# Optimization experiments

Hardware: AMD Instinct MI355X
Metric: run time of the kernel (lower is better)

Reference implementation:

```python
import jax, jax.numpy as jnp
from jax import lax
import numpy as np

B, C, H, W = 32, 1, 224, 224
F, KS = 64, 7

def setup_inputs() -> dict:
    key = jax.random.key(0)
    k1, k2 = jax.random.split(key)
    x = jax.random.normal(k1, (B, C, H, W), dtype=jnp.float32)
    # torch.rand -> uniform [0,1)
    kernel = jax.random.uniform(k2, (F, KS, KS), dtype=jnp.float32)
    return {"input": x, "kernel": kernel}

def reference(input, kernel):
    # Original: zero-pad by k//2 on all sides, then for each output pixel
    # out[b, f, i, j] = sum(patch[b, 0] * kernel[f]) -> single-input-channel conv.
    ks = kernel.shape[-1]
    pad = ks // 2
    w = kernel[:, None, :, :]  # [F, 1, ks, ks] in OIHW
    out = lax.conv_general_dilated(
        input, w,
        window_strides=(1, 1),
        padding=[(pad, pad), (pad, pad)],
        dimension_numbers=("NCHW", "OIHW", "NCHW"),
    )
    return out  # [B, F, H, W]
```

## Files before the change

kernel.cpp:

```cpp
#include <hip/hip_runtime.h>


#define TILE   32
#define HALO   3
#define LTILE  (TILE + 2 * HALO)
#define H_     224
#define W_     224
#define B_     32
#define F_     64
#define KS_    7

__global__ __launch_bounds__(256)
void Conv_58394375356438_kernel(const float* __restrict__ in,
                                const float* __restrict__ wt,
                                float* __restrict__ out)
{
    __shared__ float tile[LTILE * LTILE];

    const int blk = blockIdx.x;
    const int tx  = blk % (W_ / TILE);
    const int ty  = (blk / (W_ / TILE)) % (H_ / TILE);
    const int b   = blk / ((W_ / TILE) * (H_ / TILE));

    const int x0 = tx * TILE;
    const int y0 = ty * TILE;
    const float* __restrict__ inp = in + b * (H_ * W_);

    for (int i = threadIdx.x; i < LTILE * LTILE; i += 256) {
        const int ly = i / LTILE;
        const int lx = i - ly * LTILE;
        const int gy = y0 + ly - HALO;
        const int gx = x0 + lx - HALO;
        float v = 0.0f;
        if (gy >= 0 && gy < H_ && gx >= 0 && gx < W_)
            v = inp[gy * W_ + gx];
        tile[i] = v;
    }
    __syncthreads();

    const int r  = threadIdx.x >> 3;
    const int cx = (threadIdx.x & 7) * 4;

    float patch[KS_][10];
    #pragma unroll
    for (int ky = 0; ky < KS_; ++ky) {
        #pragma unroll
        for (int kx = 0; kx < 10; ++kx) {
            patch[ky][kx] = tile[(r + ky) * LTILE + cx + kx];
        }
    }

    float* __restrict__ outp = out + ((size_t)(b * F_) * H_ + (y0 + r)) * W_ + (x0 + cx);

    #pragma unroll 2
    for (int f = 0; f < F_; ++f) {
        const float* __restrict__ wf = wt + f * (KS_ * KS_);
        float acc0 = 0.0f, acc1 = 0.0f, acc2 = 0.0f, acc3 = 0.0f;
        #pragma unroll
        for (int ky = 0; ky < KS_; ++ky) {
            #pragma unroll
            for (int kx = 0; kx < KS_; ++kx) {
                const float w = wf[ky * KS_ + kx];
                acc0 = fmaf(patch[ky][kx + 0], w, acc0);
                acc1 = fmaf(patch[ky][kx + 1], w, acc1);
                acc2 = fmaf(patch[ky][kx + 2], w, acc2);
                acc3 = fmaf(patch[ky][kx + 3], w, acc3);
            }
        }
        float4 v = make_float4(acc0, acc1, acc2, acc3);
        *reinterpret_cast<float4*>(outp + (size_t)f * (H_ * W_)) = v;
    }
}

extern "C" void kernel_launch(void* const* d_in, const int* in_sizes, int n_in,
                              void* d_out, int out_size, void* d_ws, size_t ws_size,
                              hipStream_t stream)
{
    const float* in = (const float*)d_in[0];
    const float* wt = (const float*)d_in[1];
    float* out      = (float*)d_out;

    const int grid = B_ * (H_ / TILE) * (W_ / TILE);
    Conv_58394375356438_kernel<<<grid, 256, 0, stream>>>(in, wt, out);
}
```

Measured before the change: 527.3 us.

## Use fp16 dot2 packed MACs with LDS weights and split filters across blocks

After: 442.0 us. 16.2% less time.

```diff
diff --git a/kernel.cpp b/kernel.cpp
--- a/kernel.cpp
+++ b/kernel.cpp
@@ -1,34 +1,50 @@
 #include <hip/hip_runtime.h>
 
 
-#define TILE   32
-#define HALO   3
-#define LTILE  (TILE + 2 * HALO)
-#define H_     224
-#define W_     224
-#define B_     32
-#define F_     64
-#define KS_    7
+#define TILE    32
+#define HALO    3
+#define LTY     (TILE + 2 * HALO)
+#define LTX     40
+#define H_      224
+#define W_      224
+#define B_      32
+#define F_      64
+#define FB_     32
+#define KS_     7
+
+typedef _Float16 half2_t __attribute__((ext_vector_type(2)));
+
+__device__ __forceinline__ float dot2(half2_t a, half2_t b, float c) {
+#if __has_builtin(__builtin_amdgcn_fdot2)
+    return __builtin_amdgcn_fdot2(a, b, c, false);
+#else
+    return c + (float)a.x * (float)b.x + (float)a.y * (float)b.y;
+#endif
+}
 
 __global__ __launch_bounds__(256)
 void Conv_58394375356438_kernel(const float* __restrict__ in,
                                 const float* __restrict__ wt,
                                 float* __restrict__ out)
 {
-    __shared__ float tile[LTILE * LTILE];
+    __shared__ float   tile[LTY * LTX];
+    __shared__ half2_t w2lds[FB_ * 32];
 
-    const int blk = blockIdx.x;
-    const int tx  = blk % (W_ / TILE);
-    const int ty  = (blk / (W_ / TILE)) % (H_ / TILE);
-    const int b   = blk / ((W_ / TILE) * (H_ / TILE));
+    const int blk   = blockIdx.x;
+    const int fhalf = blk & 1;
+    const int rest  = blk >> 1;
+    const int tx    = rest % (W_ / TILE);
+    const int ty    = (rest / (W_ / TILE)) % (H_ / TILE);
+    const int b     = rest / ((W_ / TILE) * (H_ / TILE));
 
     const int x0 = tx * TILE;
     const int y0 = ty * TILE;
+    const int fb = fhalf * FB_;
     const float* __restrict__ inp = in + b * (H_ * W_);
 
-    for (int i = threadIdx.x; i < LTILE * LTILE; i += 256) {
-        const int ly = i / LTILE;
-        const int lx = i - ly * LTILE;
+    for (int i = threadIdx.x; i < LTY * LTX; i += 256) {
+        const int ly = i / LTX;
+        const int lx = i - ly * LTX;
         const int gy = y0 + ly - HALO;
         const int gx = x0 + lx - HALO;
         float v = 0.0f;
@@ -36,38 +52,60 @@
             v = inp[gy * W_ + gx];
         tile[i] = v;
     }
+
+    for (int idx = threadIdx.x; idx < FB_ * 28; idx += 256) {
+        const int f   = idx / 28;
+        const int t   = idx - f * 28;
+        const int row = t >> 2;
+        const int j   = t & 3;
+        const int kx  = 2 * j;
+        const float* wg = wt + (fb + f) * (KS_ * KS_) + row * KS_ + kx;
+        const float w0 = wg[0];
+        const float w1 = (kx + 1 < KS_) ? wg[1] : 0.0f;
+        half2_t h;
+        h.x = (_Float16)w0;
+        h.y = (_Float16)w1;
+        w2lds[f * 32 + t] = h;
+    }
     __syncthreads();
 
     const int r  = threadIdx.x >> 3;
     const int cx = (threadIdx.x & 7) * 4;
 
-    float patch[KS_][10];
+    half2_t pairs[KS_][10];
     #pragma unroll
     for (int ky = 0; ky < KS_; ++ky) {
+        const int base = (r + ky) * LTX + cx;
+        float c[11];
         #pragma unroll
-        for (int kx = 0; kx < 10; ++kx) {
-            patch[ky][kx] = tile[(r + ky) * LTILE + cx + kx];
+        for (int s = 0; s < 11; ++s) c[s] = tile[base + s];
+        #pragma unroll
+        for (int s = 0; s < 10; ++s) {
+            half2_t h;
+            h.x = (_Float16)c[s];
+            h.y = (_Float16)c[s + 1];
+            pairs[ky][s] = h;
         }
     }
 
-    float* __restrict__ outp = out + ((size_t)(b * F_) * H_ + (y0 + r)) * W_ + (x0 + cx);
+    float* __restrict__ outp =
+        out + ((size_t)(b * F_ + fb) * H_ + (y0 + r)) * W_ + (x0 + cx);
 
-    #pragma unroll 2
-    for (int f = 0; f < F_; ++f) {
-        const float* __restrict__ wf = wt + f * (KS_ * KS_);
-        float acc0 = 0.0f, acc1 = 0.0f, acc2 = 0.0f, acc3 = 0.0f;
+    for (int f = 0; f < FB_; ++f) {
+        const half2_t* __restrict__ wf = &w2lds[f * 32];
+        float a0 = 0.0f, a1 = 0.0f, a2 = 0.0f, a3 = 0.0f;
         #pragma unroll
         for (int ky = 0; ky < KS_; ++ky) {
             #pragma unroll
-            for (int kx = 0; kx < KS_; ++kx) {
-                const float w = wf[ky * KS_ + kx];
-                acc0 = fmaf(patch[ky][kx + 0], w, acc0);
-                acc1 = fmaf(patch[ky][kx + 1], w, acc1);
-                acc2 = fmaf(patch[ky][kx + 2], w, acc2);
-                acc3 = fmaf(patch[ky][kx + 3], w, acc3);
+            for (int j = 0; j < 4; ++j) {
+                const half2_t w = wf[ky * 4 + j];
+                a0 = dot2(pairs[ky][0 + 2 * j], w, a0);
+                a1 = dot2(pairs[ky][1 + 2 * j], w, a1);
+                a2 = dot2(pairs[ky][2 + 2 * j], w, a2);
+                a3 = dot2(pairs[ky][3 + 2 * j], w, a3);
             }
         }
-        float4 v = make_float4(acc0, acc1, acc2, acc3);
+        float4 v = make_float4(a0, a1, a2, a3);
         *reinterpret_cast<float4*>(outp + (size_t)f * (H_ * W_)) = v;
     }
 }
@@ -80,6 +118,6 @@
     const float* wt = (const float*)d_in[1];
     float* out      = (float*)d_out;
 
-    const int grid = B_ * (H_ / TILE) * (W_ / TILE);
+    const int grid = B_ * (H_ / TILE) * (W_ / TILE) * (F_ / FB_);
     Conv_58394375356438_kernel<<<grid, 256, 0, stream>>>(in, wt, out);
 }
```
